# Kernel optimization log

Measured on AMD Instinct MI355X. Metric: run time of the kernel, lower is better.

## Reference

```python
import jax, jax.numpy as jnp
import numpy as np

N, C, D = 2048, 1000, 768
KNN = 5          # module default
SIGMA = 1.0      # unused by kNN affinity (matches original kNN_affinity)
BOUND_LAMBDA = 1.0
MAX_STEPS = 100


def setup_inputs() -> dict:
    key = jax.random.key(0)
    k1, k2 = jax.random.split(key)
    logits = jax.random.normal(k1, (N, C), dtype=jnp.float32) * 2.0
    feats = jax.random.normal(k2, (N, D), dtype=jnp.float32)
    return {"logits": logits, "feats": feats}


def _knn_affinity(feats, knn):
    # feats are L2-normalized, so squared euclidean dist = 2 - 2 * <xi, xj>
    n = feats.shape[0]
    sim = feats @ feats.T                                  # [N, N]
    dist = jnp.sqrt(jnp.clip(2.0 - 2.0 * sim, 0.0))        # [N, N]
    _, idx = jax.lax.top_k(-dist, knn + 1)                 # knn+1 smallest distances
    idx = idx[:, 1:]                                       # drop self (dist 0)
    W = jnp.zeros((n, n), dtype=feats.dtype)
    W = W.at[jnp.arange(n)[:, None], idx].set(1.0)
    return W


def _entropy_energy(Y, unary, pairwise, lam):
    return jnp.sum(unary * Y - lam * pairwise * Y + Y * jnp.log(jnp.clip(Y, 1e-20)))


def _laplacian_optimization(unary, kernel, lam=BOUND_LAMBDA, max_steps=MAX_STEPS):
    Y0 = jax.nn.softmax(-unary, axis=-1)

    def cond(state):
        _, _, i, done = state
        return (i < max_steps) & jnp.logical_not(done)

    def body(state):
        Y, oldE, i, _ = state
        pairwise = lam * (kernel @ Y)                      # [N, C]
        Ynew = jax.nn.softmax(pairwise - unary, axis=-1)
        E = _entropy_energy(Ynew, unary, pairwise, lam)
        done = (i > 1) & (jnp.abs(E - oldE) <= 1e-8 * jnp.abs(oldE))
        return (Ynew, E, i + 1, done)

    Y, _, _, _ = jax.lax.while_loop(
        cond, body, (Y0, jnp.float32(jnp.inf), jnp.int32(0), jnp.array(False))
    )
    return Y


def reference(logits, feats):
    probas = jax.nn.softmax(logits, axis=1)
    unary = -jnp.log(probas + 1e-10)                       # [N, C]
    f = feats / jnp.linalg.norm(feats, axis=-1, keepdims=True)
    kernel = _knn_affinity(f, KNN)                         # [N, N] binary
    kernel = 0.5 * (kernel + kernel.T)                     # force_symmetry=True
    return _laplacian_optimization(unary, kernel)
```

## Files before the change

### kernel.cpp

```cpp
#include <hip/hip_runtime.h>
#include <hip/hip_cooperative_groups.h>
#include <math.h>

namespace cg = cooperative_groups;

#define N_ 2048
#define C_ 1000
#define D_ 768
#define K_ 5
#define CAP_ 128
#define MAXS_ 100
#define LB_ 128
#define LT_ 512

typedef unsigned short ushort_t;
typedef unsigned int uint_t;

__device__ inline float bflo(uint_t v) { union { uint_t i; float f; } c; c.i = v << 16; return c.f; }
__device__ inline float bfhi(uint_t v) { union { uint_t i; float f; } c; c.i = v & 0xffff0000u; return c.f; }
__device__ inline ushort_t f2b(float f) {
    union { float f; uint_t i; } c; c.f = f;
    return (ushort_t)((c.i + 0x7fffu + ((c.i >> 16) & 1u)) >> 16);
}
__device__ inline uint_t pk(float a, float b) { return (uint_t)f2b(a) | ((uint_t)f2b(b) << 16); }

__global__ __launch_bounds__(256) void k_unary(const float* __restrict__ logits,
                                               float* __restrict__ unary) {
    const int r = blockIdx.x, tid = threadIdx.x;
    const bool act = tid < 250;
    const int c0 = tid * 4;
    __shared__ float red[256];
    float4 l = act ? *(const float4*)(logits + (size_t)r * C_ + c0)
                   : make_float4(-INFINITY, -INFINITY, -INFINITY, -INFINITY);
    float m = fmaxf(fmaxf(l.x, l.y), fmaxf(l.z, l.w));
    red[tid] = m; __syncthreads();
    for (int s = 128; s > 0; s >>= 1) { if (tid < s) red[tid] = fmaxf(red[tid], red[tid + s]); __syncthreads(); }
    m = red[0]; __syncthreads();
    float e0 = 0, e1 = 0, e2 = 0, e3 = 0, sum = 0;
    if (act) { e0 = expf(l.x - m); e1 = expf(l.y - m); e2 = expf(l.z - m); e3 = expf(l.w - m); sum = e0 + e1 + e2 + e3; }
    red[tid] = sum; __syncthreads();
    for (int s = 128; s > 0; s >>= 1) { if (tid < s) red[tid] += red[tid + s]; __syncthreads(); }
    const float S = red[0]; __syncthreads();
    if (act) {
        float4 u;
        u.x = -logf(e0 / S + 1e-10f);
        u.y = -logf(e1 / S + 1e-10f);
        u.z = -logf(e2 / S + 1e-10f);
        u.w = -logf(e3 / S + 1e-10f);
        *(float4*)(unary + (size_t)r * C_ + c0) = u;
    }
}

__global__ __launch_bounds__(256) void k_norm(const float* __restrict__ feats,
                                              float* __restrict__ fn) {
    const int r = blockIdx.x, tid = threadIdx.x;
    __shared__ float red[256];
    const float* row = feats + (size_t)r * D_;
    float ss = 0.f;
    for (int c = tid; c < D_; c += 256) { float v = row[c]; ss += v * v; }
    red[tid] = ss; __syncthreads();
    for (int s = 128; s > 0; s >>= 1) { if (tid < s) red[tid] += red[tid + s]; __syncthreads(); }
    const float n = sqrtf(red[0]); __syncthreads();
    for (int c = tid; c < D_; c += 256) fn[(size_t)r * D_ + c] = row[c] / n;
}

#define GTM 128
#define GTN 128
#define GBK 32
__global__ __launch_bounds__(256, 2) void k_gemm(const float* __restrict__ A,
                                                 float* __restrict__ Csim) {
    __shared__ float As[GBK][GTM + 4];
    __shared__ float Bs[GBK][GTN + 4];
    const int tid = threadIdx.x, tx = tid & 15, ty = tid >> 4;
    const int m0 = blockIdx.y * GTM, n0 = blockIdx.x * GTN;
    float acc[8][8] = {};
    for (int k0 = 0; k0 < D_; k0 += GBK) {
        #pragma unroll
        for (int l = 0; l < 4; l++) {
            int idx = tid + l * 256;
            int mm = idx >> 3, kk = (idx & 7) * 4;
            float4 v = *(const float4*)(A + (size_t)(m0 + mm) * D_ + k0 + kk);
            As[kk][mm] = v.x; As[kk + 1][mm] = v.y; As[kk + 2][mm] = v.z; As[kk + 3][mm] = v.w;
        }
        #pragma unroll
        for (int l = 0; l < 4; l++) {
            int idx = tid + l * 256;
            int mm = idx >> 3, kk = (idx & 7) * 4;
            float4 v = *(const float4*)(A + (size_t)(n0 + mm) * D_ + k0 + kk);
            Bs[kk][mm] = v.x; Bs[kk + 1][mm] = v.y; Bs[kk + 2][mm] = v.z; Bs[kk + 3][mm] = v.w;
        }
        __syncthreads();
        #pragma unroll
        for (int kk = 0; kk < GBK; kk++) {
            float4 a0 = *(const float4*)&As[kk][ty * 8];
            float4 a1 = *(const float4*)&As[kk][ty * 8 + 4];
            float4 b0 = *(const float4*)&Bs[kk][tx * 8];
            float4 b1 = *(const float4*)&Bs[kk][tx * 8 + 4];
            float a[8] = { a0.x, a0.y, a0.z, a0.w, a1.x, a1.y, a1.z, a1.w };
            float b[8] = { b0.x, b0.y, b0.z, b0.w, b1.x, b1.y, b1.z, b1.w };
            #pragma unroll
            for (int i = 0; i < 8; i++)
                #pragma unroll
                for (int j = 0; j < 8; j++) acc[i][j] += a[i] * b[j];
        }
        __syncthreads();
    }
    #pragma unroll
    for (int i = 0; i < 8; i++) {
        float4 s0 = make_float4(acc[i][0], acc[i][1], acc[i][2], acc[i][3]);
        float4 s1 = make_float4(acc[i][4], acc[i][5], acc[i][6], acc[i][7]);
        *(float4*)(Csim + (size_t)(m0 + ty * 8 + i) * N_ + n0 + tx * 8) = s0;
        *(float4*)(Csim + (size_t)(m0 + ty * 8 + i) * N_ + n0 + tx * 8 + 4) = s1;
    }
}

__global__ __launch_bounds__(256) void k_topk(const float* __restrict__ sim,
                                              int* __restrict__ knn) {
    const int r = blockIdx.x, tid = threadIdx.x;
    float bd[6]; int bi[6];
    #pragma unroll
    for (int k = 0; k < 6; k++) { bd[k] = INFINITY; bi[k] = 0x7fffffff; }
    const float* srow = sim + (size_t)r * N_;
    for (int j = tid; j < N_; j += 256) {
        float s = srow[j];
        float d = sqrtf(fmaxf(2.f - 2.f * s, 0.f));
        if (d < bd[5] || (d == bd[5] && j < bi[5])) {
            int k = 5;
            while (k > 0 && (d < bd[k - 1] || (d == bd[k - 1] && j < bi[k - 1]))) {
                bd[k] = bd[k - 1]; bi[k] = bi[k - 1]; k--;
            }
            bd[k] = d; bi[k] = j;
        }
    }
    __shared__ float sd[256][6];
    __shared__ int   si[256][6];
    #pragma unroll
    for (int k = 0; k < 6; k++) { sd[tid][k] = bd[k]; si[tid][k] = bi[k]; }
    __syncthreads();
    for (int s = 128; s > 0; s >>= 1) {
        if (tid < s) {
            float md[6]; int mi[6];
            int p = 0, q = 0;
            #pragma unroll
            for (int k = 0; k < 6; k++) {
                float d1 = sd[tid][p], d2 = sd[tid + s][q];
                int i1 = si[tid][p], i2 = si[tid + s][q];
                bool take1 = (d1 < d2) || (d1 == d2 && i1 < i2);
                if (take1) { md[k] = d1; mi[k] = i1; p++; } else { md[k] = d2; mi[k] = i2; q++; }
            }
            #pragma unroll
            for (int k = 0; k < 6; k++) { sd[tid][k] = md[k]; si[tid][k] = mi[k]; }
        }
        __syncthreads();
    }
    if (tid < K_) knn[(size_t)r * K_ + tid] = si[0][1 + tid];
}

__global__ __launch_bounds__(256) void k_scatter(const int* __restrict__ knn,
                                                 int* __restrict__ indeg,
                                                 int* __restrict__ inlist) {
    const int i = blockIdx.x * 256 + threadIdx.x;
    if (i >= N_) return;
    #pragma unroll
    for (int k = 0; k < K_; k++) {
        const int j = knn[i * K_ + k];
        const int pos = atomicAdd(&indeg[j], 1);
        if (pos < CAP_) inlist[(size_t)j * CAP_ + pos] = i;
    }
}

__global__ __launch_bounds__(256) void k_sortin(const int* __restrict__ indeg,
                                                int* __restrict__ inlist) {
    const int j = blockIdx.x * 256 + threadIdx.x;
    if (j >= N_) return;
    int* L = inlist + (size_t)j * CAP_;
    const int cnt = min(indeg[j], CAP_);
    for (int a = 1; a < cnt; a++) {
        const int key = L[a];
        int b = a - 1;
        while (b >= 0 && L[b] > key) { L[b + 1] = L[b]; b--; }
        L[b + 1] = key;
    }
}

__global__ __launch_bounds__(LT_) void k_lame(
    const float* __restrict__ unary, const int* __restrict__ knn,
    const int* __restrict__ indeg, const int* __restrict__ inlist,
    ushort_t* __restrict__ YA, ushort_t* __restrict__ YB,
    float* __restrict__ partials, int* __restrict__ flag,
    float* __restrict__ out)
{
    cg::grid_group grid = cg::this_grid();
    const int tid = threadIdx.x;
    const int wave = tid >> 6, lane = tid & 63;
    const int rbase = blockIdx.x * 16 + wave * 2;
    const int c0 = lane * 16;
    const bool msk0 = lane <= 62;
    const bool msk1 = lane <= 61;

    __shared__ int nb[16][K_ + CAP_ + 3];
    __shared__ int cnts[16];
    #pragma unroll
    for (int rr = 0; rr < 2; rr++) {
        const int w = wave * 2 + rr, r = rbase + rr;
        if (lane == 0) cnts[w] = K_ + min(indeg[r], CAP_);
        if (lane < K_) nb[w][lane] = knn[r * K_ + lane];
        for (int t = lane; t < CAP_; t += 64) nb[w][K_ + t] = inlist[(size_t)r * CAP_ + t];
    }
    __syncthreads();
    const int cnt2[2] = { cnts[wave * 2], cnts[wave * 2 + 1] };

    float u[2][16];
    #pragma unroll
    for (int rr = 0; rr < 2; rr++) {
        const float* up = unary + (size_t)(rbase + rr) * C_ + c0;
        float4 a = *(const float4*)(up);
        float4 b = *(const float4*)(up + 4);
        float4 c = *(const float4*)(up + 8);
        float4 d = *(const float4*)(up + 12);
        u[rr][0] = a.x; u[rr][1] = a.y; u[rr][2] = a.z; u[rr][3] = a.w;
        u[rr][4] = b.x; u[rr][5] = b.y; u[rr][6] = b.z; u[rr][7] = b.w;
        u[rr][8] = c.x; u[rr][9] = c.y; u[rr][10] = c.z; u[rr][11] = c.w;
        u[rr][12] = d.x; u[rr][13] = d.y; u[rr][14] = d.z; u[rr][15] = d.w;
    }

    auto gather = [&](const ushort_t* __restrict__ src, int rr, float* acc) {
        const int w = wave * 2 + rr, cn = cnt2[rr];
        auto acc16 = [&](uint4 p, uint4 q) {
            acc[0] += bflo(p.x); acc[1] += bfhi(p.x); acc[2] += bflo(p.y); acc[3] += bfhi(p.y);
            acc[4] += bflo(p.z); acc[5] += bfhi(p.z); acc[6] += bflo(p.w); acc[7] += bfhi(p.w);
            acc[8] += bflo(q.x); acc[9] += bfhi(q.x); acc[10] += bflo(q.y); acc[11] += bfhi(q.y);
            acc[12] += bflo(q.z); acc[13] += bfhi(q.z); acc[14] += bflo(q.w); acc[15] += bfhi(q.w);
        };
        int t = 0;
        for (; t + 2 <= cn; t += 2) {
            const int n0 = nb[w][t], n1 = nb[w][t + 1];
            const uint4 p0 = *(const uint4*)(src + (size_t)n0 * C_ + c0);
            const uint4 p1 = *(const uint4*)(src + (size_t)n0 * C_ + c0 + 8);
            const uint4 q0 = *(const uint4*)(src + (size_t)n1 * C_ + c0);
            const uint4 q1 = *(const uint4*)(src + (size_t)n1 * C_ + c0 + 8);
            acc16(p0, p1); acc16(q0, q1);
        }
        if (t < cn) {
            const int n0 = nb[w][t];
            const uint4 p0 = *(const uint4*)(src + (size_t)n0 * C_ + c0);
            const uint4 p1 = *(const uint4*)(src + (size_t)n0 * C_ + c0 + 8);
            acc16(p0, p1);
        }
    };

    auto smax = [&](int rr, const float* acc, ushort_t* __restrict__ dst) -> float {
        const int r = rbase + rr;
        float z[16];
        #pragma unroll
        for (int k = 0; k < 16; k++) z[k] = 0.5f * acc[k] - u[rr][k];
        float mm = -INFINITY;
        #pragma unroll
        for (int k = 0; k < 8; k++) mm = fmaxf(mm, msk0 ? z[k] : -INFINITY);
        #pragma unroll
        for (int k = 8; k < 16; k++) mm = fmaxf(mm, msk1 ? z[k] : -INFINITY);
        #pragma unroll
        for (int o = 32; o > 0; o >>= 1) mm = fmaxf(mm, __shfl_xor(mm, o));
        float e[16];
        float s = 0.f;
        #pragma unroll
        for (int k = 0; k < 8; k++) { e[k] = msk0 ? expf(z[k] - mm) : 0.f; s += e[k]; }
        #pragma unroll
        for (int k = 8; k < 16; k++) { e[k] = msk1 ? expf(z[k] - mm) : 0.f; s += e[k]; }
        #pragma unroll
        for (int o = 32; o > 0; o >>= 1) s += __shfl_xor(s, o);
        const float inv = 1.f / s;
        if (msk0) {
            uint4 w;
            w.x = pk(e[0] * inv, e[1] * inv); w.y = pk(e[2] * inv, e[3] * inv);
            w.z = pk(e[4] * inv, e[5] * inv); w.w = pk(e[6] * inv, e[7] * inv);
            *(uint4*)(dst + (size_t)r * C_ + c0) = w;
        }
        if (msk1) {
            uint4 w;
            w.x = pk(e[8] * inv, e[9] * inv); w.y = pk(e[10] * inv, e[11] * inv);
            w.z = pk(e[12] * inv, e[13] * inv); w.w = pk(e[14] * inv, e[15] * inv);
            *(uint4*)(dst + (size_t)r * C_ + c0 + 8) = w;
        }
        return -(mm + logf(s));
    };

    {
        float zacc[16];
        #pragma unroll
        for (int k = 0; k < 16; k++) zacc[k] = 0.f;
        smax(0, zacc, YA);
        smax(1, zacc, YA);
    }
    if (blockIdx.x == 0 && tid == 0) { flag[0] = 0; flag[1] = 0; }
    grid.sync();

    float oldE = INFINITY;
    const ushort_t* fin = YB;
    for (int it = 0; it < MAXS_; ++it) {
        const ushort_t* src = (it & 1) ? YB : YA;
        ushort_t* dst = (it & 1) ? YA : YB;
        float acc0[16], acc1[16];
        #pragma unroll
        for (int k = 0; k < 16; k++) { acc0[k] = 0.f; acc1[k] = 0.f; }
        gather(src, 0, acc0);
        gather(src, 1, acc1);
        const float E0 = smax(0, acc0, dst);
        const float E1 = smax(1, acc1, dst);
        if (lane == 0) {
            partials[(size_t)(it & 1) * N_ + rbase] = E0;
            partials[(size_t)(it & 1) * N_ + rbase + 1] = E1;
        }
        grid.sync();
        if (blockIdx.x == 0 && wave == 0) {
            const float* P = partials + (size_t)(it & 1) * N_;
            float e = 0.f;
            #pragma unroll
            for (int q = 0; q < 32; q += 4) {
                float4 v = *(const float4*)(P + lane * 32 + q);
                e += ((v.x + v.y) + v.z) + v.w;
            }
            #pragma unroll
            for (int o = 32; o > 0; o >>= 1) e += __shfl_xor(e, o);
            const bool done = (it > 1) && (fabsf(e - oldE) <= 1e-8f * fabsf(oldE));
            oldE = e;
            if (lane == 0) flag[it & 1] = done ? 1 : 0;
        }
        fin = dst;
        if (((volatile const int*)flag)[(it + 1) & 1]) break;
    }

    #pragma unroll
    for (int rr = 0; rr < 2; rr++) {
        const int r = rbase + rr;
        #pragma unroll
        for (int q = 0; q < 4; q++) {
            if (c0 + q * 4 + 3 < C_) {
                const uint2 w = *(const uint2*)(fin + (size_t)r * C_ + c0 + q * 4);
                float4 o;
                o.x = bflo(w.x); o.y = bfhi(w.x); o.z = bflo(w.y); o.w = bfhi(w.y);
                *(float4*)(out + (size_t)r * C_ + c0 + q * 4) = o;
            }
        }
    }
}

extern "C" void kernel_launch(void* const* d_in, const int* in_sizes, int n_in,
                              void* d_out, int out_size, void* d_ws, size_t ws_size,
                              hipStream_t stream) {
    const float* logits = (const float*)d_in[0];
    const float* feats  = (const float*)d_in[1];
    float* out = (float*)d_out;
    char* ws = (char*)d_ws;

    size_t off = 0;
    auto alloc = [&](size_t b) { size_t o = off; off += (b + 255) & ~(size_t)255; return o; };
    float* unary   = (float*)(ws + alloc((size_t)N_ * C_ * 4));
    float* fn      = (float*)(ws + alloc((size_t)N_ * D_ * 4));
    float* sim     = (float*)(ws + alloc((size_t)N_ * N_ * 4));
    int*   knn     = (int*)(ws + alloc((size_t)N_ * K_ * 4));
    int*   indeg   = (int*)(ws + alloc((size_t)N_ * 4));
    int*   inlist  = (int*)(ws + alloc((size_t)N_ * CAP_ * 4));
    float* partials= (float*)(ws + alloc((size_t)2 * N_ * 4));
    int*   flag    = (int*)(ws + alloc(256));
    if (off > ws_size) return;

    ushort_t* YA = (ushort_t*)sim;
    ushort_t* YB = YA + (size_t)N_ * C_;

    k_unary  <<<N_, 256, 0, stream>>>(logits, unary);
    k_norm   <<<N_, 256, 0, stream>>>(feats, fn);
    k_gemm   <<<dim3(N_ / GTN, N_ / GTM), 256, 0, stream>>>(fn, sim);
    k_topk   <<<N_, 256, 0, stream>>>(sim, knn);
    (void)hipMemsetAsync(indeg, 0, (size_t)N_ * 4, stream);
    k_scatter<<<(N_ + 255) / 256, 256, 0, stream>>>(knn, indeg, inlist);
    k_sortin <<<(N_ + 255) / 256, 256, 0, stream>>>(indeg, inlist);

    const float* p_unary = unary;
    const int* p_knn = knn;
    const int* p_indeg = indeg;
    const int* p_inlist = inlist;
    ushort_t* p_YA = YA;
    ushort_t* p_YB = YB;
    float* p_part = partials;
    int* p_flag = flag;
    float* p_out = out;
    void* args[] = { &p_unary, &p_knn, &p_indeg, &p_inlist, &p_YA, &p_YB, &p_part, &p_flag, &p_out };
    (void)hipLaunchCooperativeKernel((void*)k_lame, dim3(LB_), dim3(LT_), args, 0, stream);
}
```

Baseline: 405.2 us.

## Fuse unary, scatter and in-list sort into cooperative kernel; retile GEMM to 512 threads

Drops the separate unary-softmax, memset, scatter and sort kernels. That work moves into the cooperative LAME kernel: it zeroes indeg, scatters the in-edges between two grid syncs, insertion-sorts the neighbour lists in shared memory, and computes the unary term from logits with wave shuffles. The similarity GEMM now runs 512 threads per block with an 8x4 register tile per thread. The aim is to cut kernel launch overhead and the unary buffer's round trip through memory, at the cost of two extra grid-wide syncs and serial sorting by one lane per row.

New measurement: 381.1 us. 1.06x faster.

```diff
diff --git a/kernel.cpp b/kernel.cpp
--- a/kernel.cpp
+++ b/kernel.cpp
@@ -23,33 +23,6 @@
     return (ushort_t)((c.i + 0x7fffu + ((c.i >> 16) & 1u)) >> 16);
 }
 __device__ inline uint_t pk(float a, float b) { return (uint_t)f2b(a) | ((uint_t)f2b(b) << 16); }
-
-__global__ __launch_bounds__(256) void k_unary(const float* __restrict__ logits,
-                                               float* __restrict__ unary) {
-    const int r = blockIdx.x, tid = threadIdx.x;
-    const bool act = tid < 250;
-    const int c0 = tid * 4;
-    __shared__ float red[256];
-    float4 l = act ? *(const float4*)(logits + (size_t)r * C_ + c0)
-                   : make_float4(-INFINITY, -INFINITY, -INFINITY, -INFINITY);
-    float m = fmaxf(fmaxf(l.x, l.y), fmaxf(l.z, l.w));
-    red[tid] = m; __syncthreads();
-    for (int s = 128; s > 0; s >>= 1) { if (tid < s) red[tid] = fmaxf(red[tid], red[tid + s]); __syncthreads(); }
-    m = red[0]; __syncthreads();
-    float e0 = 0, e1 = 0, e2 = 0, e3 = 0, sum = 0;
-    if (act) { e0 = expf(l.x - m); e1 = expf(l.y - m); e2 = expf(l.z - m); e3 = expf(l.w - m); sum = e0 + e1 + e2 + e3; }
-    red[tid] = sum; __syncthreads();
-    for (int s = 128; s > 0; s >>= 1) { if (tid < s) red[tid] += red[tid + s]; __syncthreads(); }
-    const float S = red[0]; __syncthreads();
-    if (act) {
-        float4 u;
-        u.x = -logf(e0 / S + 1e-10f);
-        u.y = -logf(e1 / S + 1e-10f);
-        u.z = -logf(e2 / S + 1e-10f);
-        u.w = -logf(e3 / S + 1e-10f);
-        *(float4*)(unary + (size_t)r * C_ + c0) = u;
-    }
-}
 
 __global__ __launch_bounds__(256) void k_norm(const float* __restrict__ feats,
                                               float* __restrict__ fn) {
@@ -67,24 +40,26 @@
 #define GTM 128
 #define GTN 128
 #define GBK 32
-__global__ __launch_bounds__(256, 2) void k_gemm(const float* __restrict__ A,
+__global__ __launch_bounds__(512, 2) void k_gemm(const float* __restrict__ A,
                                                  float* __restrict__ Csim) {
     __shared__ float As[GBK][GTM + 4];
     __shared__ float Bs[GBK][GTN + 4];
-    const int tid = threadIdx.x, tx = tid & 15, ty = tid >> 4;
+    const int tid = threadIdx.x;
+    const int tx = tid & 31;
+    const int ty = tid >> 5;
     const int m0 = blockIdx.y * GTM, n0 = blockIdx.x * GTN;
-    float acc[8][8] = {};
+    float acc[8][4] = {};
     for (int k0 = 0; k0 < D_; k0 += GBK) {
         #pragma unroll
-        for (int l = 0; l < 4; l++) {
-            int idx = tid + l * 256;
+        for (int l = 0; l < 2; l++) {
+            int idx = tid + l * 512;
             int mm = idx >> 3, kk = (idx & 7) * 4;
             float4 v = *(const float4*)(A + (size_t)(m0 + mm) * D_ + k0 + kk);
             As[kk][mm] = v.x; As[kk + 1][mm] = v.y; As[kk + 2][mm] = v.z; As[kk + 3][mm] = v.w;
         }
         #pragma unroll
-        for (int l = 0; l < 4; l++) {
-            int idx = tid + l * 256;
+        for (int l = 0; l < 2; l++) {
+            int idx = tid + l * 512;
             int mm = idx >> 3, kk = (idx & 7) * 4;
             float4 v = *(const float4*)(A + (size_t)(n0 + mm) * D_ + k0 + kk);
             Bs[kk][mm] = v.x; Bs[kk + 1][mm] = v.y; Bs[kk + 2][mm] = v.z; Bs[kk + 3][mm] = v.w;
@@ -94,23 +69,20 @@
         for (int kk = 0; kk < GBK; kk++) {
             float4 a0 = *(const float4*)&As[kk][ty * 8];
             float4 a1 = *(const float4*)&As[kk][ty * 8 + 4];
-            float4 b0 = *(const float4*)&Bs[kk][tx * 8];
-            float4 b1 = *(const float4*)&Bs[kk][tx * 8 + 4];
+            float4 bv = *(const float4*)&Bs[kk][tx * 4];
             float a[8] = { a0.x, a0.y, a0.z, a0.w, a1.x, a1.y, a1.z, a1.w };
-            float b[8] = { b0.x, b0.y, b0.z, b0.w, b1.x, b1.y, b1.z, b1.w };
+            float b[4] = { bv.x, bv.y, bv.z, bv.w };
             #pragma unroll
             for (int i = 0; i < 8; i++)
                 #pragma unroll
-                for (int j = 0; j < 8; j++) acc[i][j] += a[i] * b[j];
+                for (int j = 0; j < 4; j++) acc[i][j] += a[i] * b[j];
         }
         __syncthreads();
     }
     #pragma unroll
     for (int i = 0; i < 8; i++) {
-        float4 s0 = make_float4(acc[i][0], acc[i][1], acc[i][2], acc[i][3]);
-        float4 s1 = make_float4(acc[i][4], acc[i][5], acc[i][6], acc[i][7]);
-        *(float4*)(Csim + (size_t)(m0 + ty * 8 + i) * N_ + n0 + tx * 8) = s0;
-        *(float4*)(Csim + (size_t)(m0 + ty * 8 + i) * N_ + n0 + tx * 8 + 4) = s1;
+        float4 st = make_float4(acc[i][0], acc[i][1], acc[i][2], acc[i][3]);
+        *(float4*)(Csim + (size_t)(m0 + ty * 8 + i) * N_ + n0 + tx * 4) = st;
     }
 }
 
@@ -156,36 +128,9 @@
     if (tid < K_) knn[(size_t)r * K_ + tid] = si[0][1 + tid];
 }
 
-__global__ __launch_bounds__(256) void k_scatter(const int* __restrict__ knn,
-                                                 int* __restrict__ indeg,
-                                                 int* __restrict__ inlist) {
-    const int i = blockIdx.x * 256 + threadIdx.x;
-    if (i >= N_) return;
-    #pragma unroll
-    for (int k = 0; k < K_; k++) {
-        const int j = knn[i * K_ + k];
-        const int pos = atomicAdd(&indeg[j], 1);
-        if (pos < CAP_) inlist[(size_t)j * CAP_ + pos] = i;
-    }
-}
-
-__global__ __launch_bounds__(256) void k_sortin(const int* __restrict__ indeg,
-                                                int* __restrict__ inlist) {
-    const int j = blockIdx.x * 256 + threadIdx.x;
-    if (j >= N_) return;
-    int* L = inlist + (size_t)j * CAP_;
-    const int cnt = min(indeg[j], CAP_);
-    for (int a = 1; a < cnt; a++) {
-        const int key = L[a];
-        int b = a - 1;
-        while (b >= 0 && L[b] > key) { L[b + 1] = L[b]; b--; }
-        L[b + 1] = key;
-    }
-}
-
 __global__ __launch_bounds__(LT_) void k_lame(
-    const float* __restrict__ unary, const int* __restrict__ knn,
-    const int* __restrict__ indeg, const int* __restrict__ inlist,
+    const float* __restrict__ logits, const int* __restrict__ knn,
+    int* __restrict__ indeg, int* __restrict__ inlist,
     ushort_t* __restrict__ YA, ushort_t* __restrict__ YB,
     float* __restrict__ partials, int* __restrict__ flag,
     float* __restrict__ out)
@@ -198,6 +143,19 @@
     const bool msk0 = lane <= 62;
     const bool msk1 = lane <= 61;
 
+    if (tid < 16) indeg[blockIdx.x * 16 + tid] = 0;
+    grid.sync();
+    if (tid < 16) {
+        const int i = blockIdx.x * 16 + tid;
+        #pragma unroll
+        for (int k = 0; k < K_; k++) {
+            const int j = knn[i * K_ + k];
+            const int pos = atomicAdd(&indeg[j], 1);
+            if (pos < CAP_) inlist[(size_t)j * CAP_ + pos] = i;
+        }
+    }
+    grid.sync();
+
     __shared__ int nb[16][K_ + CAP_ + 3];
     __shared__ int cnts[16];
     #pragma unroll
@@ -208,20 +166,50 @@
         for (int t = lane; t < CAP_; t += 64) nb[w][K_ + t] = inlist[(size_t)r * CAP_ + t];
     }
     __syncthreads();
+    if (lane < 2) {
+        const int w = wave * 2 + lane;
+        int* L = &nb[w][K_];
+        const int cn = cnts[w] - K_;
+        for (int a = 1; a < cn; a++) {
+            const int key = L[a];
+            int b = a - 1;
+            while (b >= 0 && L[b] > key) { L[b + 1] = L[b]; b--; }
+            L[b + 1] = key;
+        }
+    }
+    __syncthreads();
     const int cnt2[2] = { cnts[wave * 2], cnts[wave * 2 + 1] };
 
     float u[2][16];
     #pragma unroll
     for (int rr = 0; rr < 2; rr++) {
-        const float* up = unary + (size_t)(rbase + rr) * C_ + c0;
-        float4 a = *(const float4*)(up);
-        float4 b = *(const float4*)(up + 4);
-        float4 c = *(const float4*)(up + 8);
-        float4 d = *(const float4*)(up + 12);
-        u[rr][0] = a.x; u[rr][1] = a.y; u[rr][2] = a.z; u[rr][3] = a.w;
-        u[rr][4] = b.x; u[rr][5] = b.y; u[rr][6] = b.z; u[rr][7] = b.w;
-        u[rr][8] = c.x; u[rr][9] = c.y; u[rr][10] = c.z; u[rr][11] = c.w;
-        u[rr][12] = d.x; u[rr][13] = d.y; u[rr][14] = d.z; u[rr][15] = d.w;
+        const float* lp = logits + (size_t)(rbase + rr) * C_;
+        float l[16];
+        #pragma unroll
+        for (int q = 0; q < 4; q++) {
+            const int off = c0 + q * 4;
+            const int ao = (off + 3 < C_) ? off : 0;
+            float4 v = *(const float4*)(lp + ao);
+            l[q * 4 + 0] = v.x; l[q * 4 + 1] = v.y; l[q * 4 + 2] = v.z; l[q * 4 + 3] = v.w;
+        }
+        float mm = -INFINITY;
+        #pragma unroll
+        for (int k = 0; k < 8; k++) mm = fmaxf(mm, msk0 ? l[k] : -INFINITY);
+        #pragma unroll
+        for (int k = 8; k < 16; k++) mm = fmaxf(mm, msk1 ? l[k] : -INFINITY);
+        #pragma unroll
+        for (int o = 32; o > 0; o >>= 1) mm = fmaxf(mm, __shfl_xor(mm, o));
+        float e[16];
+        float s = 0.f;
+        #pragma unroll
+        for (int k = 0; k < 8; k++) { e[k] = msk0 ? expf(l[k] - mm) : 0.f; s += e[k]; }
+        #pragma unroll
+        for (int k = 8; k < 16; k++) { e[k] = msk1 ? expf(l[k] - mm) : 0.f; s += e[k]; }
+        #pragma unroll
+        for (int o = 32; o > 0; o >>= 1) s += __shfl_xor(s, o);
+        const float inv = 1.f / s;
+        #pragma unroll
+        for (int k = 0; k < 16; k++) u[rr][k] = -logf(e[k] * inv + 1e-10f);
     }
 
     auto gather = [&](const ushort_t* __restrict__ src, int rr, float* acc) {
@@ -355,7 +343,6 @@
 
     size_t off = 0;
     auto alloc = [&](size_t b) { size_t o = off; off += (b + 255) & ~(size_t)255; return o; };
-    float* unary   = (float*)(ws + alloc((size_t)N_ * C_ * 4));
     float* fn      = (float*)(ws + alloc((size_t)N_ * D_ * 4));
     float* sim     = (float*)(ws + alloc((size_t)N_ * N_ * 4));
     int*   knn     = (int*)(ws + alloc((size_t)N_ * K_ * 4));
@@ -368,23 +355,19 @@
     ushort_t* YA = (ushort_t*)sim;
     ushort_t* YB = YA + (size_t)N_ * C_;
 
-    k_unary  <<<N_, 256, 0, stream>>>(logits, unary);
     k_norm   <<<N_, 256, 0, stream>>>(feats, fn);
-    k_gemm   <<<dim3(N_ / GTN, N_ / GTM), 256, 0, stream>>>(fn, sim);
+    k_gemm   <<<dim3(N_ / GTN, N_ / GTM), 512, 0, stream>>>(fn, sim);
     k_topk   <<<N_, 256, 0, stream>>>(sim, knn);
-    (void)hipMemsetAsync(indeg, 0, (size_t)N_ * 4, stream);
-    k_scatter<<<(N_ + 255) / 256, 256, 0, stream>>>(knn, indeg, inlist);
-    k_sortin <<<(N_ + 255) / 256, 256, 0, stream>>>(indeg, inlist);
-
-    const float* p_unary = unary;
+
+    const float* p_logits = logits;
     const int* p_knn = knn;
-    const int* p_indeg = indeg;
-    const int* p_inlist = inlist;
+    int* p_indeg = indeg;
+    int* p_inlist = inlist;
     ushort_t* p_YA = YA;
     ushort_t* p_YB = YB;
     float* p_part = partials;
     int* p_flag = flag;
     float* p_out = out;
-    void* args[] = { &p_unary, &p_knn, &p_indeg, &p_inlist, &p_YA, &p_YB, &p_part, &p_flag, &p_out };
+    void* args[] = { &p_logits, &p_knn, &p_indeg, &p_inlist, &p_YA, &p_YB, &p_part, &p_flag, &p_out };
     (void)hipLaunchCooperativeKernel((void*)k_lame, dim3(LB_), dim3(LT_), args, 0, stream);
 }
```
